# Optimization experiments

Measured on AMD Instinct MI355X. Metric: run time of the kernel, lower is better.

## Reference

```python
import jax, jax.numpy as jnp
import numpy as np

D_EMBED = 2048
N_HEAD = 16
HEAD_DIM = D_EMBED // N_HEAD
B, S = 4, 2048


def setup_inputs() -> dict:
    key = jax.random.key(0)
    ks = jax.random.split(key, 6)
    s = 0.02
    x = jax.random.normal(ks[0], (B, S, D_EMBED), dtype=jnp.float32)
    attention_mask = jnp.ones((B, S), dtype=bool)
    Wq = jax.random.normal(ks[1], (D_EMBED, D_EMBED), dtype=jnp.float32) * s
    Wk = jax.random.normal(ks[2], (D_EMBED, D_EMBED), dtype=jnp.float32) * s
    Wv = jax.random.normal(ks[3], (D_EMBED, D_EMBED), dtype=jnp.float32) * s
    Wo = jax.random.normal(ks[4], (D_EMBED, D_EMBED), dtype=jnp.float32) * s
    bq = jnp.zeros((D_EMBED,), jnp.float32)
    bk = jnp.zeros((D_EMBED,), jnp.float32)
    bv = jnp.zeros((D_EMBED,), jnp.float32)
    bo = jnp.zeros((D_EMBED,), jnp.float32)
    return {"x": x, "attention_mask": attention_mask,
            "Wq": Wq, "bq": bq, "Wk": Wk, "bk": bk,
            "Wv": Wv, "bv": bv, "Wo": Wo, "bo": bo}


def reference(x, attention_mask, Wq, bq, Wk, bk, Wv, bv, Wo, bo):
    bsz, seq_len, _ = x.shape

    def split_heads(t):  # [B,S,D] -> [B,H,S,hd]
        return t.reshape(bsz, seq_len, N_HEAD, HEAD_DIM).transpose(0, 2, 1, 3)

    q = split_heads(x @ Wq + bq)
    k = split_heads(x @ Wk + bk)
    v = split_heads(x @ Wv + bv)

    scale = 1.0 / np.sqrt(HEAD_DIM).astype(np.float32)
    scores = jnp.einsum('bhqd,bhkd->bhqk', q, k) * scale  # [B,H,S,S]

    # causal (past_len = 0, query_len = total_len = S) combined with key padding mask
    causal = jnp.tril(jnp.ones((seq_len, seq_len), dtype=bool))  # [S,S]
    mask = causal[None, None, :, :] & attention_mask[:, None, None, :]
    neg = jnp.finfo(scores.dtype).min
    scores = jnp.where(mask, scores, neg)

    att = jax.nn.softmax(scores, axis=-1)  # dropout p=0.0 -> identity
    out = jnp.einsum('bhqk,bhkd->bhqd', att, v)
    out = out.transpose(0, 2, 1, 3).reshape(bsz, seq_len, D_EMBED)
    return out @ Wo + bo
```

## Files before the change

### kernel.cpp

```cpp
#include <hip/hip_runtime.h>
#include <cstdint>
#include <cstddef>


#define D_EMBED 2048
#define NHEAD   16
#define HDIM    128
#define BATCH   4
#define SEQ     2048
#define MROWS   (BATCH*SEQ)

typedef __attribute__((ext_vector_type(8))) short bf16x8;
typedef __attribute__((ext_vector_type(4))) float f32x4;

__device__ __forceinline__ short f2bf(float f) {
  union { float f; uint32_t u; } v; v.f = f;
  uint32_t r = v.u + 0x7fffu + ((v.u >> 16) & 1u);
  return (short)(r >> 16);
}

__device__ __forceinline__ void async_copy16(void* lds, const void* gmem) {
  __builtin_amdgcn_global_load_lds(
      (__attribute__((address_space(1))) void*)gmem,
      (__attribute__((address_space(3))) void*)lds, 16, 0, 0);
}

__global__ __launch_bounds__(256) void cvt_x(const float* __restrict__ x,
                                             short* __restrict__ xb) {
  int i = blockIdx.x * 256 + threadIdx.x;
  float4 v = reinterpret_cast<const float4*>(x)[i];
  short4 o;
  o.x = f2bf(v.x); o.y = f2bf(v.y); o.z = f2bf(v.z); o.w = f2bf(v.w);
  reinterpret_cast<short4*>(xb)[i] = o;
}

struct TransArgs { const float* src[4]; short* dst[4]; };

__global__ __launch_bounds__(256) void transpose_w(TransArgs ta) {
  const int z = blockIdx.z;
  const float* W = ta.src[z];
  short* Wt = ta.dst[z];
  __shared__ float tile[32][33];
  int bx = blockIdx.x * 32, by = blockIdx.y * 32;
  int tx = threadIdx.x & 31, ty = threadIdx.x >> 5;
#pragma unroll
  for (int r = ty; r < 32; r += 8)
    tile[r][tx] = W[(size_t)(by + r) * D_EMBED + bx + tx];
  __syncthreads();
#pragma unroll
  for (int r = ty; r < 32; r += 8)
    Wt[(size_t)(bx + r) * D_EMBED + by + tx] = f2bf(tile[tx][r]);
}

struct GemmArgs {
  const short* A;
  const short* Bt[3];
  const float* bias[3];
  void*        out[3];
  float        scale[3];
  int          mode[3];
};

__global__ __launch_bounds__(256, 2) void gemm128(GemmArgs ga) {
  const int z = blockIdx.z;
  const short* __restrict__ A  = ga.A;
  const short* __restrict__ Bt = ga.Bt[z];
  const int row0 = blockIdx.y * 128;
  const int col0 = blockIdx.x * 128;

  __shared__ short Als[128 * 32];
  __shared__ short Bls[128 * 32];

  const int tid  = threadIdx.x;
  const int lane = tid & 63, wave = tid >> 6;
  const int lr   = lane & 15, quad = lane >> 4;
  const int wm   = wave >> 1, wn = wave & 1;

  const int cg   = ((lane & 3) ^ ((lane >> 3) & 3)) * 8;
  const int rln  = lane >> 2;
  const int psw  = (quad ^ ((lr >> 1) & 3)) * 8;

  f32x4 acc[4][4] = {};

  for (int k0 = 0; k0 < D_EMBED; k0 += 32) {
#pragma unroll
    for (int t = 0; t < 2; ++t) {
      int r0 = wave * 32 + t * 16;
      async_copy16(&Als[r0 * 32],
                   A + (size_t)(row0 + r0 + rln) * D_EMBED + k0 + cg);
    }
#pragma unroll
    for (int t = 0; t < 2; ++t) {
      int r0 = wave * 32 + t * 16;
      async_copy16(&Bls[r0 * 32],
                   Bt + (size_t)(col0 + r0 + rln) * D_EMBED + k0 + cg);
    }
    __syncthreads();

    bf16x8 av[4], bv[4];
#pragma unroll
    for (int mi = 0; mi < 4; ++mi)
      av[mi] = *reinterpret_cast<const bf16x8*>(&Als[(wm * 64 + mi * 16 + lr) * 32 + psw]);
#pragma unroll
    for (int ni = 0; ni < 4; ++ni)
      bv[ni] = *reinterpret_cast<const bf16x8*>(&Bls[(wn * 64 + ni * 16 + lr) * 32 + psw]);
#pragma unroll
    for (int mi = 0; mi < 4; ++mi)
#pragma unroll
      for (int ni = 0; ni < 4; ++ni)
        acc[mi][ni] = __builtin_amdgcn_mfma_f32_16x16x32_bf16(av[mi], bv[ni], acc[mi][ni], 0, 0, 0);
    __syncthreads();
  }

  const float* __restrict__ bias = ga.bias[z];
  const int mode = ga.mode[z];
  const float scl = ga.scale[z];
  if (mode != 2) {
#pragma unroll
    for (int mi = 0; mi < 4; ++mi)
#pragma unroll
      for (int ni = 0; ni < 4; ++ni) {
        int n = col0 + wn * 64 + ni * 16 + lr;
        float bias_n = bias[n];
#pragma unroll
        for (int i = 0; i < 4; ++i) {
          int m = row0 + wm * 64 + mi * 16 + quad * 4 + i;
          float v = (acc[mi][ni][i] + bias_n) * scl;
          if (mode == 0) ((short*)ga.out[z])[(size_t)m * D_EMBED + n] = f2bf(v);
          else           ((float*)ga.out[z])[(size_t)m * D_EMBED + n] = v;
        }
      }
  } else {
    short* Vt = (short*)ga.out[z];
#pragma unroll
    for (int ni = 0; ni < 4; ++ni) {
      int n = col0 + wn * 64 + ni * 16 + lr;
      int h = n >> 7, dd = n & (HDIM - 1);
      float bias_n = bias[n];
#pragma unroll
      for (int mi = 0; mi < 4; ++mi)
#pragma unroll
        for (int i = 0; i < 4; ++i) {
          int m = row0 + wm * 64 + mi * 16 + quad * 4 + i;
          int b = m >> 11, t = m & (SEQ - 1);
          Vt[(size_t)((b * NHEAD + h) * HDIM + dd) * SEQ + t] = f2bf(acc[mi][ni][i] + bias_n);
        }
    }
  }
}

#define COMPUTE_STRIP(qf, o, l_i, qrow, diag, t0)                               \
  {                                                                             \
    f32x4 sc[4] = {};                                                           \
    _Pragma("unroll")                                                           \
    for (int nt = 0; nt < 4; ++nt)                                              \
      _Pragma("unroll")                                                         \
      for (int ks = 0; ks < 4; ++ks) {                                          \
        bf16x8 kf = *reinterpret_cast<const bf16x8*>(                           \
            &Kls[(nt * 16 + lr) * 128 + (((ks * 4 + quad) ^ lr) * 8)]);         \
        sc[nt] = __builtin_amdgcn_mfma_f32_16x16x32_bf16(qf[ks], kf, sc[nt], 0, 0, 0); \
      }                                                                         \
    if (diag) {                                                                 \
      _Pragma("unroll")                                                         \
      for (int nt = 0; nt < 4; ++nt) {                                          \
        int t = (t0) + nt * 16 + lr;                                            \
        _Pragma("unroll")                                                       \
        for (int i = 0; i < 4; ++i)                                             \
          if (t > (qrow) + quad * 4 + i) sc[nt][i] = -1e30f;                    \
      }                                                                         \
    }                                                                           \
    _Pragma("unroll")                                                           \
    for (int nt = 0; nt < 4; ++nt)                                              \
      _Pragma("unroll")                                                         \
      for (int i = 0; i < 4; ++i) {                                             \
        float p = exp2f(sc[nt][i]);                                             \
        l_i[i] += p;                                                            \
        Pls[wave][(quad * 4 + i) * 72 + nt * 16 + lr] = f2bf(p);                \
      }                                                                         \
    _Pragma("unroll")                                                           \
    for (int n2 = 0; n2 < 8; ++n2)                                              \
      _Pragma("unroll")                                                         \
      for (int k2 = 0; k2 < 2; ++k2) {                                          \
        bf16x8 pf = *reinterpret_cast<const bf16x8*>(                           \
            &Pls[wave][lr * 72 + k2 * 32 + quad * 8]);                          \
        bf16x8 vf = *reinterpret_cast<const bf16x8*>(                           \
            &Vls[(n2 * 16 + lr) * 64 + (((k2 * 4 + quad) ^ (lr & 7)) * 8)]);    \
        o[n2] = __builtin_amdgcn_mfma_f32_16x16x32_bf16(pf, vf, o[n2], 0, 0, 0);\
      }                                                                         \
  }

#define FINALIZE_STRIP(o, l_i, qrow)                                            \
  {                                                                             \
    _Pragma("unroll")                                                           \
    for (int off = 1; off < 16; off <<= 1)                                      \
      _Pragma("unroll")                                                         \
      for (int i = 0; i < 4; ++i) l_i[i] += __shfl_xor(l_i[i], off);            \
    float inv_l[4];                                                             \
    _Pragma("unroll")                                                           \
    for (int i = 0; i < 4; ++i) inv_l[i] = 1.0f / l_i[i];                       \
    short* obase = O + (size_t)(b * SEQ + (qrow)) * D_EMBED + h * HDIM;         \
    _Pragma("unroll")                                                           \
    for (int n2 = 0; n2 < 8; ++n2)                                              \
      _Pragma("unroll")                                                         \
      for (int i = 0; i < 4; ++i)                                               \
        obase[(size_t)(quad * 4 + i) * D_EMBED + n2 * 16 + lr] =                \
            f2bf(o[n2][i] * inv_l[i]);                                          \
  }

__global__ __launch_bounds__(256, 2) void flash_attn(const short* __restrict__ Q,
                                                     const short* __restrict__ K,
                                                     const short* __restrict__ Vt,
                                                     short* __restrict__ O) {
  __shared__ short Kls[64 * 128];
  __shared__ short Vls[128 * 64];
  __shared__ short Pls[4][16 * 72];

  const int lane = threadIdx.x & 63, wave = threadIdx.x >> 6;
  const int lr = lane & 15, quad = lane >> 4;
  const int b = blockIdx.z, h = blockIdx.y;
  const int qb_lo = blockIdx.x;
  const int qb_hi = 31 - qb_lo;
  const int qrow_lo = qb_lo * 64 + wave * 16;
  const int qrow_hi = qb_hi * 64 + wave * 16;

  const int krow = lane >> 4;
  const int kcg_base = lane & 15;
  const int vrow = lane >> 3;
  const int vcg = ((lane & 7) ^ (lane >> 3)) * 8;

  bf16x8 qf_lo[4], qf_hi[4];
  {
    const short* qp0 = Q + (size_t)(b * SEQ + qrow_lo + lr) * D_EMBED + h * HDIM;
    const short* qp1 = Q + (size_t)(b * SEQ + qrow_hi + lr) * D_EMBED + h * HDIM;
#pragma unroll
    for (int ks = 0; ks < 4; ++ks) {
      qf_lo[ks] = *reinterpret_cast<const bf16x8*>(qp0 + ks * 32 + quad * 8);
      qf_hi[ks] = *reinterpret_cast<const bf16x8*>(qp1 + ks * 32 + quad * 8);
    }
  }

  f32x4 o_lo[8] = {}, o_hi[8] = {};
  float l_lo[4] = {}, l_hi[4] = {};

  const short* Kbase  = K + (size_t)b * SEQ * D_EMBED + h * HDIM;
  const short* Vtbase = Vt + (size_t)((b * NHEAD + h) * HDIM) * SEQ;

  for (int tt = 0; tt <= qb_hi; ++tt) {
    const int t0 = tt * 64;
#pragma unroll
    for (int s = 0; s < 4; ++s) {
      int r0 = wave * 16 + s * 4;
      int r  = r0 + krow;
      int cg = (kcg_base ^ ((s * 4 + krow) & 15)) * 8;
      async_copy16(&Kls[r0 * 128],
                   Kbase + (size_t)(t0 + r) * D_EMBED + cg);
    }
#pragma unroll
    for (int s = 0; s < 4; ++s) {
      int r0 = wave * 32 + s * 8;
      int r  = r0 + vrow;
      async_copy16(&Vls[r0 * 64],
                   Vtbase + (size_t)r * SEQ + t0 + vcg);
    }
    __syncthreads();

    COMPUTE_STRIP(qf_hi, o_hi, l_hi, qrow_hi, tt == qb_hi, t0);
    if (tt <= qb_lo)
      COMPUTE_STRIP(qf_lo, o_lo, l_lo, qrow_lo, tt == qb_lo, t0);
    __syncthreads();
  }

  FINALIZE_STRIP(o_hi, l_hi, qrow_hi);
  FINALIZE_STRIP(o_lo, l_lo, qrow_lo);
}

extern "C" void kernel_launch(void* const* d_in, const int* in_sizes, int n_in,
                              void* d_out, int out_size, void* d_ws, size_t ws_size,
                              hipStream_t stream) {
  const float* x  = (const float*)d_in[0];
  const float* Wq = (const float*)d_in[2];
  const float* bq = (const float*)d_in[3];
  const float* Wk = (const float*)d_in[4];
  const float* bk = (const float*)d_in[5];
  const float* Wv = (const float*)d_in[6];
  const float* bv = (const float*)d_in[7];
  const float* Wo = (const float*)d_in[8];
  const float* bo = (const float*)d_in[9];

  char* ws = (char*)d_ws;
  const size_t MB32 = (size_t)MROWS * D_EMBED * 2;
  const size_t WSZ  = (size_t)D_EMBED * D_EMBED * 2;
  short* Xb   = (short*)(ws);
  short* Wqt  = (short*)(ws + MB32);
  short* Wkt  = (short*)(ws + MB32 + WSZ);
  short* Wvt  = (short*)(ws + MB32 + 2 * WSZ);
  short* Wot  = (short*)(ws + MB32 + 3 * WSZ);
  short* Qb   = (short*)(ws + 2 * MB32);
  short* Kb   = (short*)(ws + 3 * MB32);
  short* Vtb  = (short*)(ws + 4 * MB32);
  short* attn = Xb;

  const float scale2 = 0.08838834764831845f * 1.4426950408889634f;

  cvt_x<<<(MROWS * D_EMBED) / 4 / 256, 256, 0, stream>>>(x, Xb);

  TransArgs ta{{Wq, Wk, Wv, Wo}, {Wqt, Wkt, Wvt, Wot}};
  transpose_w<<<dim3(64, 64, 4), 256, 0, stream>>>(ta);

  GemmArgs ga;
  ga.A = Xb;
  ga.Bt[0] = Wqt; ga.Bt[1] = Wkt; ga.Bt[2] = Wvt;
  ga.bias[0] = bq; ga.bias[1] = bk; ga.bias[2] = bv;
  ga.out[0] = Qb; ga.out[1] = Kb; ga.out[2] = Vtb;
  ga.scale[0] = scale2; ga.scale[1] = 1.f; ga.scale[2] = 1.f;
  ga.mode[0] = 0; ga.mode[1] = 0; ga.mode[2] = 2;
  gemm128<<<dim3(D_EMBED / 128, MROWS / 128, 3), 256, 0, stream>>>(ga);

  flash_attn<<<dim3(16, NHEAD, BATCH), 256, 0, stream>>>(Qb, Kb, Vtb, attn);

  GemmArgs gb;
  gb.A = attn;
  gb.Bt[0] = Wot; gb.Bt[1] = Wot; gb.Bt[2] = Wot;
  gb.bias[0] = bo; gb.bias[1] = bo; gb.bias[2] = bo;
  gb.out[0] = d_out; gb.out[1] = d_out; gb.out[2] = d_out;
  gb.scale[0] = 1.f; gb.scale[1] = 1.f; gb.scale[2] = 1.f;
  gb.mode[0] = 1; gb.mode[1] = 1; gb.mode[2] = 1;
  gemm128<<<dim3(D_EMBED / 128, MROWS / 128, 1), 256, 0, stream>>>(gb);
}
```

Baseline: 646.6 us.

## Replace 128x128 GEMM with double-buffered 256x256 tile, 8-wave pipelined kernel

The projection GEMMs move from 128x128 tiles with a single-buffered K=32 loop to 256x256 tiles run by 512 threads. The K loop uses K=64 stages with double-buffered LDS, interleaving async global-to-LDS copies with MFMA quadrants under explicit waitcnt and barrier control and raised wave priority. It also remaps workgroup IDs for L2 locality and swizzles the LDS layout. The aim is to raise arithmetic intensity and hide memory latency, at the cost of more registers and LDS per block, fewer blocks in flight, and fragile hand-tuned synchronisation.

```diff
diff --git a/kernel.cpp b/kernel.cpp
--- a/kernel.cpp
+++ b/kernel.cpp
@@ -61,70 +61,148 @@
   int          mode[3];
 };
 
-__global__ __launch_bounds__(256, 2) void gemm128(GemmArgs ga) {
+__global__ __launch_bounds__(512, 2) void gemm256(GemmArgs ga) {
   const int z = blockIdx.z;
   const short* __restrict__ A  = ga.A;
   const short* __restrict__ Bt = ga.Bt[z];
-  const int row0 = blockIdx.y * 128;
-  const int col0 = blockIdx.x * 128;
-
-  __shared__ short Als[128 * 32];
-  __shared__ short Bls[128 * 32];
+
+  const int lin  = blockIdx.y * 8 + blockIdx.x;
+  const int wg   = (lin & 7) * 32 + (lin >> 3);
+  const int col0 = (wg & 7) * 256;
+  const int row0 = (wg >> 3) * 256;
+
+  __shared__ __align__(16) short As[2][2][2][64 * 64];
+  __shared__ __align__(16) short Bs[2][2][128 * 64];
 
   const int tid  = threadIdx.x;
-  const int lane = tid & 63, wave = tid >> 6;
+  const int lane = tid & 63, w = tid >> 6;
   const int lr   = lane & 15, quad = lane >> 4;
-  const int wm   = wave >> 1, wn = wave & 1;
-
-  const int cg   = ((lane & 3) ^ ((lane >> 3) & 3)) * 8;
-  const int rln  = lane >> 2;
-  const int psw  = (quad ^ ((lr >> 1) & 3)) * 8;
-
-  f32x4 acc[4][4] = {};
-
-  for (int k0 = 0; k0 < D_EMBED; k0 += 32) {
-#pragma unroll
-    for (int t = 0; t < 2; ++t) {
-      int r0 = wave * 32 + t * 16;
-      async_copy16(&Als[r0 * 32],
-                   A + (size_t)(row0 + r0 + rln) * D_EMBED + k0 + cg);
-    }
-#pragma unroll
-    for (int t = 0; t < 2; ++t) {
-      int r0 = wave * 32 + t * 16;
-      async_copy16(&Bls[r0 * 32],
-                   Bt + (size_t)(col0 + r0 + rln) * D_EMBED + k0 + cg);
-    }
-    __syncthreads();
-
-    bf16x8 av[4], bv[4];
-#pragma unroll
-    for (int mi = 0; mi < 4; ++mi)
-      av[mi] = *reinterpret_cast<const bf16x8*>(&Als[(wm * 64 + mi * 16 + lr) * 32 + psw]);
-#pragma unroll
-    for (int ni = 0; ni < 4; ++ni)
-      bv[ni] = *reinterpret_cast<const bf16x8*>(&Bls[(wn * 64 + ni * 16 + lr) * 32 + psw]);
-#pragma unroll
-    for (int mi = 0; mi < 4; ++mi)
-#pragma unroll
-      for (int ni = 0; ni < 4; ++ni)
-        acc[mi][ni] = __builtin_amdgcn_mfma_f32_16x16x32_bf16(av[mi], bv[ni], acc[mi][ni], 0, 0, 0);
-    __syncthreads();
-  }
+  const int wm   = w >> 2, wn = w & 3;
+  const int lr8  = lane >> 3;
+  const int srccol = ((lane & 7) ^ (((lane >> 5) & 1) << 1)) * 8;
+  const int csw = (quad ^ (((lr >> 2) & 1) << 1)) * 8;
+
+  bf16x8 av[4][2], bv[2][2];
+  f32x4 acc[8][4] = {};
+
+#define STAGE_A(buf, Mh, kk) do {                                              \
+    _Pragma("unroll")                                                          \
+    for (int j = 0; j < 2; ++j)                                                \
+      async_copy16(&As[buf][Mh][j][w * 512],                                   \
+          A + (size_t)(row0 + j * 128 + (Mh) * 64 + w * 8 + lr8) * D_EMBED +   \
+              (kk) + srccol);                                                  \
+  } while (0)
+
+#define STAGE_B(buf, Nh, kk) do {                                              \
+    _Pragma("unroll")                                                          \
+    for (int j = 0; j < 2; ++j) {                                              \
+      int fr_ = j * 64 + w * 8 + lr8;                                          \
+      async_copy16(&Bs[buf][Nh][(j * 64 + w * 8) * 64],                        \
+          Bt + (size_t)(col0 + (fr_ >> 5) * 64 + (Nh) * 32 + (fr_ & 31)) *     \
+                  D_EMBED + (kk) + srccol);                                    \
+    }                                                                          \
+  } while (0)
+
+#define LOAD_A(buf, Mh) do {                                                   \
+    _Pragma("unroll")                                                          \
+    for (int t = 0; t < 4; ++t) {                                              \
+      const short* ap_ = &As[buf][Mh][wm][(t * 16 + lr) * 64];                 \
+      av[t][0] = *reinterpret_cast<const bf16x8*>(ap_ + csw);                  \
+      av[t][1] = *reinterpret_cast<const bf16x8*>(ap_ + csw + 32);             \
+    }                                                                          \
+  } while (0)
+
+#define LOAD_B(buf, Nh) do {                                                   \
+    _Pragma("unroll")                                                          \
+    for (int u = 0; u < 2; ++u) {                                              \
+      const short* bp_ = &Bs[buf][Nh][(wn * 32 + u * 16 + lr) * 64];           \
+      bv[u][0] = *reinterpret_cast<const bf16x8*>(bp_ + csw);                  \
+      bv[u][1] = *reinterpret_cast<const bf16x8*>(bp_ + csw + 32);             \
+    }                                                                          \
+  } while (0)
+
+#define MFMA_Q(Mh, Nh) do {                                                    \
+    _Pragma("unroll")                                                          \
+    for (int ks = 0; ks < 2; ++ks)                                             \
+      _Pragma("unroll")                                                        \
+      for (int t = 0; t < 4; ++t)                                              \
+        _Pragma("unroll")                                                      \
+        for (int u = 0; u < 2; ++u)                                            \
+          acc[(Mh) * 4 + t][(Nh) * 2 + u] =                                    \
+              __builtin_amdgcn_mfma_f32_16x16x32_bf16(                         \
+                  av[t][ks], bv[u][ks], acc[(Mh) * 4 + t][(Nh) * 2 + u],       \
+                  0, 0, 0);                                                    \
+  } while (0)
+
+#define PHASE_TAIL(Mh, Nh) do {                                                \
+    __builtin_amdgcn_s_barrier();                                              \
+    asm volatile("s_waitcnt lgkmcnt(0)" ::: "memory");                         \
+    __builtin_amdgcn_sched_barrier(0);                                         \
+    __builtin_amdgcn_s_setprio(1);                                             \
+    MFMA_Q(Mh, Nh);                                                            \
+    __builtin_amdgcn_s_setprio(0);                                             \
+    __builtin_amdgcn_s_barrier();                                              \
+  } while (0)
+
+  STAGE_A(0, 0, 0);  STAGE_B(0, 1, 0);  STAGE_A(0, 1, 0);  STAGE_B(0, 0, 0);
+  STAGE_A(1, 0, 64); STAGE_B(1, 1, 64); STAGE_A(1, 1, 64);
+  asm volatile("s_waitcnt vmcnt(6)" ::: "memory");
+  __builtin_amdgcn_s_barrier();
+
+#pragma unroll 1
+  for (int it = 0; it < 16; ++it) {
+    const int kc = it * 128;
+    LOAD_A(0, 0); LOAD_B(0, 0);
+    STAGE_B(1, 0, kc + 64);
+    asm volatile("s_waitcnt lgkmcnt(8)" ::: "memory");
+    PHASE_TAIL(0, 0);
+    LOAD_B(0, 1);
+    STAGE_A(0, 0, kc + 128);
+    PHASE_TAIL(0, 1);
+    LOAD_A(0, 1);
+    STAGE_B(0, 1, kc + 128);
+    PHASE_TAIL(1, 1);
+    LOAD_B(0, 0);
+    STAGE_A(0, 1, kc + 128);
+    asm volatile("s_waitcnt vmcnt(6)" ::: "memory");
+    PHASE_TAIL(1, 0);
+    LOAD_A(1, 0); LOAD_B(1, 0);
+    STAGE_B(0, 0, kc + 128);
+    asm volatile("s_waitcnt lgkmcnt(8)" ::: "memory");
+    PHASE_TAIL(0, 0);
+    LOAD_B(1, 1);
+    STAGE_A(1, 0, kc + 192);
+    PHASE_TAIL(0, 1);
+    LOAD_A(1, 1);
+    STAGE_B(1, 1, kc + 192);
+    PHASE_TAIL(1, 1);
+    LOAD_B(1, 0);
+    STAGE_A(1, 1, kc + 192);
+    asm volatile("s_waitcnt vmcnt(6)" ::: "memory");
+    PHASE_TAIL(1, 0);
+  }
+  asm volatile("s_waitcnt vmcnt(0)" ::: "memory");
+
+#undef STAGE_A
+#undef STAGE_B
+#undef LOAD_A
+#undef LOAD_B
+#undef MFMA_Q
+#undef PHASE_TAIL
 
   const float* __restrict__ bias = ga.bias[z];
   const int mode = ga.mode[z];
   const float scl = ga.scale[z];
   if (mode != 2) {
 #pragma unroll
-    for (int mi = 0; mi < 4; ++mi)
+    for (int mi = 0; mi < 8; ++mi)
 #pragma unroll
       for (int ni = 0; ni < 4; ++ni) {
         int n = col0 + wn * 64 + ni * 16 + lr;
         float bias_n = bias[n];
 #pragma unroll
         for (int i = 0; i < 4; ++i) {
-          int m = row0 + wm * 64 + mi * 16 + quad * 4 + i;
+          int m = row0 + wm * 128 + mi * 16 + quad * 4 + i;
           float v = (acc[mi][ni][i] + bias_n) * scl;
           if (mode == 0) ((short*)ga.out[z])[(size_t)m * D_EMBED + n] = f2bf(v);
           else           ((float*)ga.out[z])[(size_t)m * D_EMBED + n] = v;
@@ -138,10 +216,10 @@
       int h = n >> 7, dd = n & (HDIM - 1);
       float bias_n = bias[n];
 #pragma unroll
-      for (int mi = 0; mi < 4; ++mi)
+      for (int mi = 0; mi < 8; ++mi)
 #pragma unroll
         for (int i = 0; i < 4; ++i) {
-          int m = row0 + wm * 64 + mi * 16 + quad * 4 + i;
+          int m = row0 + wm * 128 + mi * 16 + quad * 4 + i;
           int b = m >> 11, t = m & (SEQ - 1);
           Vt[(size_t)((b * NHEAD + h) * HDIM + dd) * SEQ + t] = f2bf(acc[mi][ni][i] + bias_n);
         }
@@ -314,7 +392,7 @@
   ga.out[0] = Qb; ga.out[1] = Kb; ga.out[2] = Vtb;
   ga.scale[0] = scale2; ga.scale[1] = 1.f; ga.scale[2] = 1.f;
   ga.mode[0] = 0; ga.mode[1] = 0; ga.mode[2] = 2;
-  gemm128<<<dim3(D_EMBED / 128, MROWS / 128, 3), 256, 0, stream>>>(ga);
+  gemm256<<<dim3(D_EMBED / 256, MROWS / 256, 3), 512, 0, stream>>>(ga);
 
   flash_attn<<<dim3(16, NHEAD, BATCH), 256, 0, stream>>>(Qb, Kb, Vtb, attn);
 
@@ -325,5 +403,5 @@
   gb.out[0] = d_out; gb.out[1] = d_out; gb.out[2] = d_out;
   gb.scale[0] = 1.f; gb.scale[1] = 1.f; gb.scale[2] = 1.f;
   gb.mode[0] = 1; gb.mode[1] = 1; gb.mode[2] = 1;
-  gemm128<<<dim3(D_EMBED / 128, MROWS / 128, 1), 256, 0, stream>>>(gb);
-}
+  gemm256<<<dim3(D_EMBED / 256, MROWS / 256, 1), 512, 0, stream>>>(gb);
+}
```

Result: faster. 611.1 us (-5.5%).
